# Kernel optimization log

Hardware: AMD Instinct MI355X
Metric: run time of the kernel (lower is better)

The kernel has to match this reference:

```python
import jax, jax.numpy as jnp
import numpy as np

H = 64  # hidden size
IN = 1  # input size


def setup_inputs() -> dict:
    key = jax.random.key(0)
    ks = jax.random.split(key, 8)
    B, T = 4096, 512
    s_ih = 1.0 / np.sqrt(H)
    return {
        "x": jax.random.normal(ks[0], (B, T, IN), dtype=jnp.float32),
        # PyTorch LSTM params, gate order (i, f, g, o)
        "W_ih": jax.random.uniform(ks[1], (4 * H, IN), jnp.float32, -s_ih, s_ih),
        "W_hh": jax.random.uniform(ks[2], (4 * H, H), jnp.float32, -s_ih, s_ih),
        "b_ih": jax.random.uniform(ks[3], (4 * H,), jnp.float32, -s_ih, s_ih),
        "b_hh": jax.random.uniform(ks[4], (4 * H,), jnp.float32, -s_ih, s_ih),
        "W_fc": jax.random.uniform(ks[5], (1, H), jnp.float32, -s_ih, s_ih),
        "b_fc": jax.random.uniform(ks[6], (1,), jnp.float32, -s_ih, s_ih),
    }


def reference(x, W_ih, W_hh, b_ih, b_hh, W_fc, b_fc):
    B = x.shape[0]
    b = b_ih + b_hh  # fused bias, [4H]

    def step(carry, xt):
        h, c = carry  # [B,H], [B,H]
        gates = xt @ W_ih.T + h @ W_hh.T + b  # [B,4H]
        i, f, g, o = jnp.split(gates, 4, axis=-1)
        i = jax.nn.sigmoid(i)
        f = jax.nn.sigmoid(f)
        g = jnp.tanh(g)
        o = jax.nn.sigmoid(o)
        c = f * c + i * g
        h = o * jnp.tanh(c)
        return (h, c), None

    h0 = jnp.zeros((B, H), dtype=x.dtype)
    c0 = jnp.zeros((B, H), dtype=x.dtype)
    xs = jnp.swapaxes(x, 0, 1)  # [T,B,IN]
    (h_last, _), _ = jax.lax.scan(step, (h0, c0), xs)
    # fc applied to out[:, -1, :] == h_last
    return h_last @ W_fc.T + b_fc  # [B,1]
```

## Files before the change

kernel.cpp:

```cpp
#include <hip/hip_runtime.h>

#define T_STEPS 512
#define BT 16
#define XSTRIDE 524
#define HSTRIDE 72

typedef __attribute__((ext_vector_type(8))) _Float16 f16x8;
typedef __attribute__((ext_vector_type(4))) _Float16 f16x4;
typedef __attribute__((ext_vector_type(4))) float f32x4;

__device__ __forceinline__ float exp2_fast(float x) {
#if __has_builtin(__builtin_amdgcn_exp2f)
    return __builtin_amdgcn_exp2f(x);
#else
    return __expf(x * 0.69314718056f);
#endif
}

#define L2E 1.44269504089f
#define C2  2.88539008178f

__global__ __launch_bounds__(256, 1) void lstm_persist(
    const float* __restrict__ x,
    const float* __restrict__ W_ih,
    const float* __restrict__ W_hh,
    const float* __restrict__ b_ih,
    const float* __restrict__ b_hh,
    const float* __restrict__ W_fc,
    const float* __restrict__ b_fc,
    float* __restrict__ out)
{
    __shared__ __align__(16) float x_lds[BT * XSTRIDE];
    __shared__ __align__(16) _Float16 hbuf[2][BT][HSTRIDE];

    const int tid  = threadIdx.x;
    const int wave = tid >> 6;
    const int lane = tid & 63;
    const int l15  = lane & 15;
    const int quad = lane >> 4;
    const int b0   = blockIdx.x * BT;

    {
        const float* xg = x + (size_t)b0 * T_STEPS;
        #pragma unroll
        for (int i = 0; i < 8; ++i) {
            int f4 = tid + i * 256;
            int b  = f4 >> 7;
            int t4 = f4 & 127;
            float4 v = reinterpret_cast<const float4*>(xg + (size_t)b * T_STEPS)[t4];
            reinterpret_cast<float4*>(&x_lds[b * XSTRIDE + t4 * 4])[0] = v;
        }
    }
    {
        _Float16* p = &hbuf[0][0][0];
        for (int i = tid; i < BT * HSTRIDE; i += 256) p[i] = (_Float16)0.f;
        if (tid < BT) {
            x_lds[tid * XSTRIDE + 512] = 0.f;
            x_lds[tid * XSTRIDE + 513] = 0.f;
            x_lds[tid * XSTRIDE + 514] = 0.f;
            x_lds[tid * XSTRIDE + 515] = 0.f;
        }
    }

    const float scg[4] = { -L2E, -L2E, -C2, -L2E };
    f16x8 Wf[4][2];
    f32x4 bias4[4], wih4[4];
    #pragma unroll
    for (int g = 0; g < 4; ++g) {
        int na = g * 64 + wave * 16 + l15;
        #pragma unroll
        for (int m = 0; m < 2; ++m) {
            const float* wr = W_hh + na * 64 + m * 32 + quad * 8;
            f16x8 a;
            #pragma unroll
            for (int j = 0; j < 8; ++j) a[j] = (_Float16)(wr[j] * scg[g]);
            Wf[g][m] = a;
        }
        #pragma unroll
        for (int r = 0; r < 4; ++r) {
            int n = g * 64 + wave * 16 + quad * 4 + r;
            bias4[g][r] = scg[g] * (b_ih[n] + b_hh[n]);
            wih4[g][r]  = scg[g] * W_ih[n];
        }
    }

    f32x4 ct4 = {0.f, 0.f, 0.f, 0.f};
    const int hoff = l15 * HSTRIDE + quad * 8;
    const int wofs = l15 * HSTRIDE + wave * 16 + quad * 4;
    const f32x4* xrow4 = reinterpret_cast<const f32x4*>(&x_lds[l15 * XSTRIDE]);

    const f32x4 vone  = {1.f, 1.f, 1.f, 1.f};
    const f32x4 vnC2  = {-C2, -C2, -C2, -C2};
    const f32x4 vC2   = {C2, C2, C2, C2};
    const f32x4 vn40  = {-40.f, -40.f, -40.f, -40.f};

    __syncthreads();

    f32x4 xq = xrow4[0];
    f32x4 iv[4];
    {
        f32x4 xv4 = {xq[0], xq[0], xq[0], xq[0]};
        #pragma unroll
        for (int g = 0; g < 4; ++g)
            iv[g] = __builtin_elementwise_fma(wih4[g], xv4, bias4[g]);
    }

    #pragma unroll 2
    for (int tg = 0; tg < T_STEPS / 4; ++tg) {
        f32x4 xqn = xrow4[tg + 1];
        #pragma unroll
        for (int u = 0; u < 4; ++u) {
            const int rb = u & 1, wb = rb ^ 1;
            const _Float16* hb = &hbuf[rb][0][0];

            f16x8 bm0 = *reinterpret_cast<const f16x8*>(hb + hoff);
            f16x8 bm1 = *reinterpret_cast<const f16x8*>(hb + hoff + 32);

            f32x4 acc[4];
            #pragma unroll
            for (int g = 0; g < 4; ++g)
                acc[g] = __builtin_amdgcn_mfma_f32_16x16x32_f16(Wf[g][0], bm0, iv[g], 0, 0, 0);
            #pragma unroll
            for (int g = 0; g < 4; ++g)
                acc[g] = __builtin_amdgcn_mfma_f32_16x16x32_f16(Wf[g][1], bm1, acc[g], 0, 0, 0);

            {
                float xn = (u < 3) ? xq[u + 1] : xqn[0];
                f32x4 xn4 = {xn, xn, xn, xn};
                #pragma unroll
                for (int g = 0; g < 4; ++g)
                    iv[g] = __builtin_elementwise_fma(wih4[g], xn4, bias4[g]);
            }

            f32x4 ei, ef, eg, eo;
            #pragma unroll
            for (int r = 0; r < 4; ++r) {
                ei[r] = exp2_fast(acc[0][r]);
                ef[r] = exp2_fast(acc[1][r]);
                eg[r] = exp2_fast(acc[2][r]);
                eo[r] = exp2_fast(acc[3][r]);
            }
            f32x4 Ai = vone + ei, Af = vone + ef, Ag = vone + eg, Ao = vone + eo;
            f32x4 P   = Ai * Ag;
            f32x4 PAF = P * Af;
            f32x4 rP;
            #pragma unroll
            for (int r = 0; r < 4; ++r) rP[r] = __builtin_amdgcn_rcpf(PAF[r]);
            f32x4 tg4 = __builtin_elementwise_fma(vnC2, eg, vC2);
            f32x4 num = __builtin_elementwise_fma(ct4, P, tg4 * Af);
            f32x4 cn  = num * rP;
            ct4 = cn;
            f32x4 mx = __builtin_elementwise_max(cn, vn40);
            f32x4 ec;
            #pragma unroll
            for (int r = 0; r < 4; ++r) ec[r] = exp2_fast(-mx[r]);
            f32x4 tc  = vone - ec;
            f32x4 den = __builtin_elementwise_fma(Ao, ec, Ao);
            f32x4 rden;
            #pragma unroll
            for (int r = 0; r < 4; ++r) rden[r] = __builtin_amdgcn_rcpf(den[r]);
            f32x4 hv = tc * rden;

            f16x4 h16 = { (_Float16)hv[0], (_Float16)hv[1],
                          (_Float16)hv[2], (_Float16)hv[3] };
            *reinterpret_cast<f16x4*>(&hbuf[wb][0][0] + wofs) = h16;

            __syncthreads();
        }
        xq = xqn;
    }

    if (tid < 16) {
        int b = tid;
        float s = b_fc[0];
        #pragma unroll 4
        for (int k = 0; k < 64; ++k) {
            s += (float)hbuf[0][b][k] * W_fc[k];
        }
        out[b0 + b] = s;
    }
}

extern "C" void kernel_launch(void* const* d_in, const int* in_sizes, int n_in,
                              void* d_out, int out_size, void* d_ws, size_t ws_size,
                              hipStream_t stream) {
    const float* x    = (const float*)d_in[0];
    const float* W_ih = (const float*)d_in[1];
    const float* W_hh = (const float*)d_in[2];
    const float* b_ih = (const float*)d_in[3];
    const float* b_hh = (const float*)d_in[4];
    const float* W_fc = (const float*)d_in[5];
    const float* b_fc = (const float*)d_in[6];
    float* out = (float*)d_out;
    const int B = in_sizes[0] / T_STEPS;
    lstm_persist<<<dim3(B / BT), dim3(256), 0, stream>>>(
        x, W_ih, W_hh, b_ih, b_hh, W_fc, b_fc, out);
}
```

Before: 261.6 us.

## Process two 16-row batch tiles per 512-thread block for wave interleaving

Doubles the batch tile to 32 rows and splits each block into two independent groups of four waves. Each group has its own h double-buffer, so two recurrent chains share each SIMD and can hide each other's MFMA and transcendental latency. It also computes the next input projection before the MFMAs and folds the final h computation into one FMA. The trade-off is that the grid halves to 128 blocks, leaving half the CUs idle, and both tiles are tied to one block-wide barrier every step.

```diff
diff --git a/kernel.cpp b/kernel.cpp
--- a/kernel.cpp
+++ b/kernel.cpp
@@ -1,7 +1,7 @@
 #include <hip/hip_runtime.h>
 
 #define T_STEPS 512
-#define BT 16
+#define BT 32
 #define XSTRIDE 524
 #define HSTRIDE 72
 
@@ -20,7 +20,7 @@
 #define L2E 1.44269504089f
 #define C2  2.88539008178f
 
-__global__ __launch_bounds__(256, 1) void lstm_persist(
+__global__ __launch_bounds__(512, 2) void lstm_persist(
     const float* __restrict__ x,
     const float* __restrict__ W_ih,
     const float* __restrict__ W_hh,
@@ -31,10 +31,12 @@
     float* __restrict__ out)
 {
     __shared__ __align__(16) float x_lds[BT * XSTRIDE];
-    __shared__ __align__(16) _Float16 hbuf[2][BT][HSTRIDE];
+    __shared__ __align__(16) _Float16 hbuf[2][2][16][HSTRIDE];
 
     const int tid  = threadIdx.x;
     const int wave = tid >> 6;
+    const int tile = wave >> 2;
+    const int w4   = wave & 3;
     const int lane = tid & 63;
     const int l15  = lane & 15;
     const int quad = lane >> 4;
@@ -44,7 +46,7 @@
         const float* xg = x + (size_t)b0 * T_STEPS;
         #pragma unroll
         for (int i = 0; i < 8; ++i) {
-            int f4 = tid + i * 256;
+            int f4 = tid + i * 512;
             int b  = f4 >> 7;
             int t4 = f4 & 127;
             float4 v = reinterpret_cast<const float4*>(xg + (size_t)b * T_STEPS)[t4];
@@ -52,13 +54,11 @@
         }
     }
     {
-        _Float16* p = &hbuf[0][0][0];
-        for (int i = tid; i < BT * HSTRIDE; i += 256) p[i] = (_Float16)0.f;
-        if (tid < BT) {
-            x_lds[tid * XSTRIDE + 512] = 0.f;
-            x_lds[tid * XSTRIDE + 513] = 0.f;
-            x_lds[tid * XSTRIDE + 514] = 0.f;
-            x_lds[tid * XSTRIDE + 515] = 0.f;
+        _Float16* p = &hbuf[0][0][0][0];
+        for (int i = tid; i < 2 * 16 * HSTRIDE; i += 512) p[i] = (_Float16)0.f;
+        if (tid < 128) {
+            int rw = tid >> 2, j = tid & 3;
+            x_lds[rw * XSTRIDE + 512 + j] = 0.f;
         }
     }
 
@@ -67,7 +67,7 @@
     f32x4 bias4[4], wih4[4];
     #pragma unroll
     for (int g = 0; g < 4; ++g) {
-        int na = g * 64 + wave * 16 + l15;
+        int na = g * 64 + w4 * 16 + l15;
         #pragma unroll
         for (int m = 0; m < 2; ++m) {
             const float* wr = W_hh + na * 64 + m * 32 + quad * 8;
@@ -78,16 +78,18 @@
         }
         #pragma unroll
         for (int r = 0; r < 4; ++r) {
-            int n = g * 64 + wave * 16 + quad * 4 + r;
+            int n = g * 64 + w4 * 16 + quad * 4 + r;
             bias4[g][r] = scg[g] * (b_ih[n] + b_hh[n]);
             wih4[g][r]  = scg[g] * W_ih[n];
         }
     }
 
     f32x4 ct4 = {0.f, 0.f, 0.f, 0.f};
+    _Float16* hb0 = &hbuf[0][tile][0][0];
+    _Float16* hb1 = &hbuf[1][tile][0][0];
     const int hoff = l15 * HSTRIDE + quad * 8;
-    const int wofs = l15 * HSTRIDE + wave * 16 + quad * 4;
-    const f32x4* xrow4 = reinterpret_cast<const f32x4*>(&x_lds[l15 * XSTRIDE]);
+    const int wofs = l15 * HSTRIDE + w4 * 16 + quad * 4;
+    const f32x4* xrow4 = reinterpret_cast<const f32x4*>(&x_lds[(tile * 16 + l15) * XSTRIDE]);
 
     const f32x4 vone  = {1.f, 1.f, 1.f, 1.f};
     const f32x4 vnC2  = {-C2, -C2, -C2, -C2};
@@ -110,27 +112,30 @@
         f32x4 xqn = xrow4[tg + 1];
         #pragma unroll
         for (int u = 0; u < 4; ++u) {
-            const int rb = u & 1, wb = rb ^ 1;
-            const _Float16* hb = &hbuf[rb][0][0];
-
-            f16x8 bm0 = *reinterpret_cast<const f16x8*>(hb + hoff);
-            f16x8 bm1 = *reinterpret_cast<const f16x8*>(hb + hoff + 32);
-
-            f32x4 acc[4];
-            #pragma unroll
-            for (int g = 0; g < 4; ++g)
-                acc[g] = __builtin_amdgcn_mfma_f32_16x16x32_f16(Wf[g][0], bm0, iv[g], 0, 0, 0);
-            #pragma unroll
-            for (int g = 0; g < 4; ++g)
-                acc[g] = __builtin_amdgcn_mfma_f32_16x16x32_f16(Wf[g][1], bm1, acc[g], 0, 0, 0);
-
+            const _Float16* hbR = (u & 1) ? hb1 : hb0;
+            _Float16*       hbW = (u & 1) ? hb0 : hb1;
+
+            f16x8 bm0 = *reinterpret_cast<const f16x8*>(hbR + hoff);
+            f16x8 bm1 = *reinterpret_cast<const f16x8*>(hbR + hoff + 32);
+
+            f32x4 ivn[4];
             {
                 float xn = (u < 3) ? xq[u + 1] : xqn[0];
                 f32x4 xn4 = {xn, xn, xn, xn};
                 #pragma unroll
                 for (int g = 0; g < 4; ++g)
-                    iv[g] = __builtin_elementwise_fma(wih4[g], xn4, bias4[g]);
+                    ivn[g] = __builtin_elementwise_fma(wih4[g], xn4, bias4[g]);
             }
+
+            f32x4 acc[4];
+            #pragma unroll
+            for (int g = 0; g < 4; ++g)
+                acc[g] = __builtin_amdgcn_mfma_f32_16x16x32_f16(Wf[g][0], bm0, iv[g], 0, 0, 0);
+            #pragma unroll
+            for (int g = 0; g < 4; ++g)
+                acc[g] = __builtin_amdgcn_mfma_f32_16x16x32_f16(Wf[g][1], bm1, acc[g], 0, 0, 0);
+            #pragma unroll
+            for (int g = 0; g < 4; ++g) iv[g] = ivn[g];
 
             f32x4 ei, ef, eg, eo;
             #pragma unroll
@@ -154,28 +159,27 @@
             f32x4 ec;
             #pragma unroll
             for (int r = 0; r < 4; ++r) ec[r] = exp2_fast(-mx[r]);
-            f32x4 tc  = vone - ec;
             f32x4 den = __builtin_elementwise_fma(Ao, ec, Ao);
             f32x4 rden;
             #pragma unroll
             for (int r = 0; r < 4; ++r) rden[r] = __builtin_amdgcn_rcpf(den[r]);
-            f32x4 hv = tc * rden;
+            f32x4 hv = __builtin_elementwise_fma(-ec, rden, rden);
 
             f16x4 h16 = { (_Float16)hv[0], (_Float16)hv[1],
                           (_Float16)hv[2], (_Float16)hv[3] };
-            *reinterpret_cast<f16x4*>(&hbuf[wb][0][0] + wofs) = h16;
+            *reinterpret_cast<f16x4*>(hbW + wofs) = h16;
 
             __syncthreads();
         }
         xq = xqn;
     }
 
-    if (tid < 16) {
+    if (tid < BT) {
         int b = tid;
         float s = b_fc[0];
         #pragma unroll 4
         for (int k = 0; k < 64; ++k) {
-            s += (float)hbuf[0][b][k] * W_fc[k];
+            s += (float)hbuf[0][b >> 4][b & 15][k] * W_fc[k];
         }
         out[b0 + b] = s;
     }
@@ -193,6 +197,6 @@
     const float* b_fc = (const float*)d_in[6];
     float* out = (float*)d_out;
     const int B = in_sizes[0] / T_STEPS;
-    lstm_persist<<<dim3(B / BT), dim3(256), 0, stream>>>(
+    lstm_persist<<<dim3(B / BT), dim3(512), 0, stream>>>(
         x, W_ih, W_hh, b_ih, b_hh, W_fc, b_fc, out);
 }
```

Result: slower. 347.6 us (+32.9%).
